# Kernel tuning notes

Hardware: AMD Instinct MI355X
Metric: run time of the kernel (lower is better)

The kernel has to match this reference:

```python
import jax, jax.numpy as jnp
import numpy as np

V, H, B, S = 32000, 2048, 128, 512
NEG_INF = -1e9

def setup_inputs() -> dict:
    key = jax.random.key(0)
    ks = jax.random.split(key, 12)
    sc = 1.0 / np.sqrt(H)
    embed = jax.random.normal(ks[0], (V, H), jnp.float32) * sc
    embed = embed.at[0].set(0.0)  # padding_idx=0
    return {
        "target_words": jax.random.randint(ks[1], (B,), 0, V),
        "hx": jax.random.normal(ks[2], (B, H), jnp.float32),
        "cx": jax.random.normal(ks[3], (B, H), jnp.float32),
        "ew_hx_list": jax.random.normal(ks[4], (S, B, H), jnp.float32),
        "ew_mask": jax.random.randint(ks[5], (S, B, 1), 0, 2).astype(jnp.int32),
        "embed": embed,
        "W_ih": jax.random.normal(ks[6], (4 * H, H), jnp.float32) * sc,
        "W_hh": jax.random.normal(ks[7], (4 * H, H), jnp.float32) * sc,
        "b_ih": jax.random.normal(ks[8], (4 * H,), jnp.float32) * sc,
        "b_hh": jax.random.normal(ks[9], (4 * H,), jnp.float32) * sc,
        "attn_W": jax.random.normal(ks[10], (H, 2 * H), jnp.float32) * sc,
        "attn_b": jax.random.normal(ks[11], (H,), jnp.float32) * sc,
    }

def reference(target_words, hx, cx, ew_hx_list, ew_mask, embed, W_ih, W_hh, b_ih, b_hh, attn_W, attn_b):
    # forward(): embedding (dropout is identity in eval) + LSTMCell step
    x = embed[target_words]                                   # [B,H]
    gates = x @ W_ih.T + b_ih + hx @ W_hh.T + b_hh            # [B,4H]
    i, f, g, o = jnp.split(gates, 4, axis=-1)                 # PyTorch gate order
    i = jax.nn.sigmoid(i); f = jax.nn.sigmoid(f); o = jax.nn.sigmoid(o)
    g = jnp.tanh(g)
    cx_new = f * cx + i * g
    hx_new = o * jnp.tanh(cx_new)                             # [B,H]
    # attention(): masked dot-score softmax over source dim 0
    scores = jnp.sum(hx_new * ew_hx_list, axis=-1, keepdims=True)  # [S,B,1]
    masked = jnp.where(ew_mask == 0, NEG_INF, scores)
    align = jax.nn.softmax(masked, axis=0)                    # [S,B,1]
    content = jnp.sum(align * ew_hx_list, axis=0)             # [B,H]
    concat = jnp.concatenate([content, hx_new], axis=1)       # [B,2H]
    hx_attention = jnp.tanh(concat @ attn_W.T + attn_b)       # [B,H]
    return hx_attention
```

## Files before the change

kernel.cpp:

```cpp
#include <hip/hip_runtime.h>
#include <math.h>

#define B 128
#define H 2048
#define S 512
#define FOURH 8192
#define LOG2E 1.4426950408889634f

typedef float  f32x4  __attribute__((ext_vector_type(4)));
typedef short  bf16x8 __attribute__((ext_vector_type(8)));
typedef unsigned short u16;
typedef unsigned short u16x8 __attribute__((ext_vector_type(8)));
typedef unsigned short u16x4 __attribute__((ext_vector_type(4)));

__device__ __forceinline__ void cvt_hilo(float x, u16& h, u16& lo) {
    unsigned int u = __float_as_uint(x);
    h = (u16)(u >> 16);
    float hf = __uint_as_float(u & 0xFFFF0000u);
    float r = x - hf;
    lo = (u16)(__float_as_uint(r) >> 16);
}

__global__ __launch_bounds__(256) void gather_convert_A0(
    const int* __restrict__ tw,
    const float* __restrict__ embed,
    const float* __restrict__ hx,
    u16* __restrict__ Ah, u16* __restrict__ Al)
{
    const int i = (blockIdx.x * 256 + threadIdx.x) * 8;
    const int b = i >> 12;
    const int col = i & 4095;
    const float* src = (col < H) ? (embed + (size_t)tw[b] * H + col)
                                 : (hx + (size_t)b * H + (col - H));
    f32x4 v0 = *(const f32x4*)(src);
    f32x4 v1 = *(const f32x4*)(src + 4);
    u16x8 hv, lv;
    #pragma unroll
    for (int j = 0; j < 4; ++j) { u16 h, l; cvt_hilo(v0[j], h, l); hv[j] = h; lv[j] = l; }
    #pragma unroll
    for (int j = 0; j < 4; ++j) { u16 h, l; cvt_hilo(v1[j], h, l); hv[4+j] = h; lv[4+j] = l; }
    *(u16x8*)(Ah + i) = hv;
    *(u16x8*)(Al + i) = lv;
}

template<int MODE>
__global__ __launch_bounds__(256) void split_gemm(
    const u16* __restrict__ Ah, const u16* __restrict__ Al,
    const float* __restrict__ W0, const float* __restrict__ W1,
    float* __restrict__ outp)
{
    constexpr int NOUT = (MODE == 0) ? FOURH : H;
    constexpr int KLEN = (MODE == 0) ? 512 : 256;
    constexpr int NITER = KLEN / 32;
    __shared__ u16 AhS[128][40];
    __shared__ u16 AlS[128][40];
    __shared__ u16 BhS[128][40];
    __shared__ u16 BlS[128][40];

    const int tid = threadIdx.x;
    const int n0 = blockIdx.x * 128;
    const int kz = blockIdx.y;
    const int kbase = kz * KLEN;
    const int sr = tid >> 1;
    const int sc = (tid & 1) * 16;
    const int wv = tid >> 6, lane = tid & 63;
    const int wr = (wv >> 1) * 64;
    const int wc = (wv & 1) * 64;
    const int frow = lane & 15, fk = (lane >> 4) * 8, crow = (lane >> 4) * 4;

    const float* Wrow;
    if (MODE == 0)
        Wrow = ((kz < 4) ? W0 : W1) + (size_t)(n0 + sr) * H + (kz & 3) * KLEN + sc;
    else
        Wrow = W0 + (size_t)(n0 + sr) * (2 * H) + kbase + sc;

    const u16* Abase = Ah + (size_t)sr * 4096 + kbase + sc;
    const u16* Lbase = Al + (size_t)sr * 4096 + kbase + sc;

    f32x4 acc[4][4];
    #pragma unroll
    for (int mi = 0; mi < 4; ++mi)
        #pragma unroll
        for (int ni = 0; ni < 4; ++ni)
            acc[mi][ni] = (f32x4){0.f, 0.f, 0.f, 0.f};

    u16x8 rah0, rah1, ral0, ral1;
    auto loadA = [&](int k0) {
        rah0 = *(const u16x8*)(Abase + k0);
        rah1 = *(const u16x8*)(Abase + k0 + 8);
        ral0 = *(const u16x8*)(Lbase + k0);
        ral1 = *(const u16x8*)(Lbase + k0 + 8);
    };
    auto writeA = [&]() {
        *(u16x8*)&AhS[sr][sc]     = rah0;
        *(u16x8*)&AhS[sr][sc + 8] = rah1;
        *(u16x8*)&AlS[sr][sc]     = ral0;
        *(u16x8*)&AlS[sr][sc + 8] = ral1;
    };
    f32x4 wX0, wX1, wX2, wX3, wY0, wY1, wY2, wY3;
    auto loadWX = [&](int k0) {
        wX0 = *(const f32x4*)(Wrow + k0);
        wX1 = *(const f32x4*)(Wrow + k0 + 4);
        wX2 = *(const f32x4*)(Wrow + k0 + 8);
        wX3 = *(const f32x4*)(Wrow + k0 + 12);
    };
    auto loadWY = [&](int k0) {
        wY0 = *(const f32x4*)(Wrow + k0);
        wY1 = *(const f32x4*)(Wrow + k0 + 4);
        wY2 = *(const f32x4*)(Wrow + k0 + 8);
        wY3 = *(const f32x4*)(Wrow + k0 + 12);
    };
    auto writeB = [&](const f32x4& b0, const f32x4& b1,
                      const f32x4& b2, const f32x4& b3) {
        u16x8 hv, lv;
        #pragma unroll
        for (int j = 0; j < 4; ++j) { u16 h, l; cvt_hilo(b0[j], h, l); hv[j] = h; lv[j] = l; }
        #pragma unroll
        for (int j = 0; j < 4; ++j) { u16 h, l; cvt_hilo(b1[j], h, l); hv[4+j] = h; lv[4+j] = l; }
        *(u16x8*)&BhS[sr][sc] = hv;
        *(u16x8*)&BlS[sr][sc] = lv;
        #pragma unroll
        for (int j = 0; j < 4; ++j) { u16 h, l; cvt_hilo(b2[j], h, l); hv[j] = h; lv[j] = l; }
        #pragma unroll
        for (int j = 0; j < 4; ++j) { u16 h, l; cvt_hilo(b3[j], h, l); hv[4+j] = h; lv[4+j] = l; }
        *(u16x8*)&BhS[sr][sc + 8] = hv;
        *(u16x8*)&BlS[sr][sc + 8] = lv;
    };
    auto computeTile = [&]() {
        bf16x8 a_h[4], a_l[4], b_h[4], b_l[4];
        #pragma unroll
        for (int mi = 0; mi < 4; ++mi) {
            a_h[mi] = *(const bf16x8*)&AhS[wr + mi * 16 + frow][fk];
            a_l[mi] = *(const bf16x8*)&AlS[wr + mi * 16 + frow][fk];
        }
        #pragma unroll
        for (int ni = 0; ni < 4; ++ni) {
            b_h[ni] = *(const bf16x8*)&BhS[wc + ni * 16 + frow][fk];
            b_l[ni] = *(const bf16x8*)&BlS[wc + ni * 16 + frow][fk];
        }
        #pragma unroll
        for (int mi = 0; mi < 4; ++mi)
            #pragma unroll
            for (int ni = 0; ni < 4; ++ni) {
                acc[mi][ni] = __builtin_amdgcn_mfma_f32_16x16x32_bf16(a_h[mi], b_h[ni], acc[mi][ni], 0, 0, 0);
                acc[mi][ni] = __builtin_amdgcn_mfma_f32_16x16x32_bf16(a_h[mi], b_l[ni], acc[mi][ni], 0, 0, 0);
                acc[mi][ni] = __builtin_amdgcn_mfma_f32_16x16x32_bf16(a_l[mi], b_h[ni], acc[mi][ni], 0, 0, 0);
            }
    };

    loadWX(0);
    loadWY(32);
    loadA(0);

    for (int ks = 0; ks < NITER; ks += 2) {
        __syncthreads();
        writeA();
        writeB(wX0, wX1, wX2, wX3);
        __syncthreads();
        loadA((ks + 1) * 32);
        if (ks + 2 < NITER) loadWX((ks + 2) * 32);
        computeTile();
        __syncthreads();
        writeA();
        writeB(wY0, wY1, wY2, wY3);
        __syncthreads();
        if (ks + 2 < NITER) loadA((ks + 2) * 32);
        if (ks + 3 < NITER) loadWY((ks + 3) * 32);
        computeTile();
    }

    #pragma unroll
    for (int mi = 0; mi < 4; ++mi)
        #pragma unroll
        for (int ni = 0; ni < 4; ++ni) {
            const int col = n0 + wc + ni * 16 + frow;
            #pragma unroll
            for (int j = 0; j < 4; ++j) {
                const int row = wr + mi * 16 + crow + j;
                outp[((size_t)kz * B + row) * NOUT + col] = acc[mi][ni][j];
            }
        }
}

__global__ __launch_bounds__(256) void lstm_cell(
    const float* __restrict__ gp,
    const float* __restrict__ cx,
    const float* __restrict__ b_ih,
    const float* __restrict__ b_hh,
    float* __restrict__ hxn,
    u16* __restrict__ Ah1, u16* __restrict__ Al1)
{
    const int t = blockIdx.x * 256 + threadIdx.x;
    const int b = t >> 9;
    const int h = (t & 511) * 4;
    const size_t PS = (size_t)B * FOURH;
    const float* g0 = gp + (size_t)b * FOURH;
    f32x4 gi = *(const f32x4*)(b_ih + h)       + *(const f32x4*)(b_hh + h);
    f32x4 gf = *(const f32x4*)(b_ih + H + h)   + *(const f32x4*)(b_hh + H + h);
    f32x4 gg = *(const f32x4*)(b_ih + 2*H + h) + *(const f32x4*)(b_hh + 2*H + h);
    f32x4 go = *(const f32x4*)(b_ih + 3*H + h) + *(const f32x4*)(b_hh + 3*H + h);
    #pragma unroll
    for (int p = 0; p < 8; ++p) {
        gi += *(const f32x4*)(g0 + p * PS + h);
        gf += *(const f32x4*)(g0 + p * PS + H + h);
        gg += *(const f32x4*)(g0 + p * PS + 2*H + h);
        go += *(const f32x4*)(g0 + p * PS + 3*H + h);
    }
    f32x4 cv = *(const f32x4*)(cx + (size_t)b * H + h);
    f32x4 hv;
    #pragma unroll
    for (int j = 0; j < 4; ++j) {
        float i_ = 1.f / (1.f + expf(-gi[j]));
        float f_ = 1.f / (1.f + expf(-gf[j]));
        float o_ = 1.f / (1.f + expf(-go[j]));
        float g_ = tanhf(gg[j]);
        float c_ = f_ * cv[j] + i_ * g_;
        hv[j] = o_ * tanhf(c_);
    }
    *(f32x4*)(hxn + (size_t)b * H + h) = hv;
    u16x4 hh, ll;
    #pragma unroll
    for (int j = 0; j < 4; ++j) { u16 a, l; cvt_hilo(hv[j], a, l); hh[j] = a; ll[j] = l; }
    *(u16x4*)(Ah1 + (size_t)b * 4096 + H + h) = hh;
    *(u16x4*)(Al1 + (size_t)b * 4096 + H + h) = ll;
}

__global__ __launch_bounds__(256) void fused_attn(
    const float* __restrict__ hxn,
    const float* __restrict__ ew,
    const int* __restrict__ mask,
    float* __restrict__ o_part,
    float* __restrict__ ml_part)
{
    __shared__ float mlbuf[4][2];
    __shared__ float obuf[4][2048];

    const int tid = threadIdx.x;
    const int b = blockIdx.x >> 2;
    const int c = blockIdx.x & 3;
    const int wv = tid >> 6;
    const int lane = tid & 63;
    const int s0 = c * 128 + wv * 32;

    unsigned long long mbits;
    {
        int mv = (lane < 32) ? mask[(s0 + lane) * B + b] : 0;
        mbits = __ballot(mv != 0);
    }

    f32x4 hxv[8];
    const float* hp = hxn + (size_t)b * H + lane * 4;
    #pragma unroll
    for (int j = 0; j < 8; ++j) hxv[j] = *(const f32x4*)(hp + j * 256);

    f32x4 o4[8];
    #pragma unroll
    for (int j = 0; j < 8; ++j) o4[j] = (f32x4){0.f, 0.f, 0.f, 0.f};
    float m2 = -3.0e38f, l = 0.f;

    const size_t SSTRIDE = (size_t)B * H;
    const float* rowp = ew + ((size_t)s0 * B + b) * H + lane * 4;

    f32x4 eva[8], evb[8];
    #pragma unroll
    for (int j = 0; j < 8; ++j) eva[j] = *(const f32x4*)(rowp + j * 256);
    #pragma unroll
    for (int j = 0; j < 8; ++j) evb[j] = *(const f32x4*)(rowp + SSTRIDE + j * 256);

    for (int pi = 0; pi < 16; ++pi) {
        f32x4 ca[8], cb[8];
        #pragma unroll
        for (int j = 0; j < 8; ++j) { ca[j] = eva[j]; cb[j] = evb[j]; }
        if (pi < 15) {
            const float* na = rowp + (size_t)(2 * pi + 2) * SSTRIDE;
            const float* nb = rowp + (size_t)(2 * pi + 3) * SSTRIDE;
            #pragma unroll
            for (int j = 0; j < 8; ++j) eva[j] = *(const f32x4*)(na + j * 256);
            #pragma unroll
            for (int j = 0; j < 8; ++j) evb[j] = *(const f32x4*)(nb + j * 256);
        }
        float pa = 0.f, pb = 0.f;
        #pragma unroll
        for (int j = 0; j < 8; ++j) {
            f32x4 ta = ca[j] * hxv[j];
            f32x4 tb = cb[j] * hxv[j];
            pa += ta[0] + ta[1] + ta[2] + ta[3];
            pb += tb[0] + tb[1] + tb[2] + tb[3];
        }
        #pragma unroll
        for (int off = 32; off; off >>= 1) {
            pa += __shfl_xor(pa, off, 64);
            pb += __shfl_xor(pb, off, 64);
        }
        const float p2a = ((mbits >> (2 * pi)) & 1) ? pa * LOG2E : -1.5e9f;
        const float p2b = ((mbits >> (2 * pi + 1)) & 1) ? pb * LOG2E : -1.5e9f;
        const float q = fmaxf(p2a, p2b);
        if (q <= m2) {
            const float ea = exp2f(p2a - m2);
            const float eb = exp2f(p2b - m2);
            l += ea + eb;
            #pragma unroll
            for (int j = 0; j < 8; ++j) o4[j] += ca[j] * ea + cb[j] * eb;
        } else {
            const float sc = exp2f(m2 - q);
            const float ea = exp2f(p2a - q);
            const float eb = exp2f(p2b - q);
            l = l * sc + ea + eb;
            #pragma unroll
            for (int j = 0; j < 8; ++j) o4[j] = o4[j] * sc + ca[j] * ea + cb[j] * eb;
            m2 = q;
        }
    }

    if (lane == 0) { mlbuf[wv][0] = m2; mlbuf[wv][1] = l; }
    __syncthreads();
    const float M = fmaxf(fmaxf(mlbuf[0][0], mlbuf[1][0]), fmaxf(mlbuf[2][0], mlbuf[3][0]));
    const float wsc = exp2f(m2 - M);
    float L = 0.f;
    #pragma unroll
    for (int w = 0; w < 4; ++w) L += mlbuf[w][1] * exp2f(mlbuf[w][0] - M);
    #pragma unroll
    for (int j = 0; j < 8; ++j)
        *(f32x4*)&obuf[wv][j * 256 + lane * 4] = o4[j] * wsc;
    __syncthreads();

    const int h0 = tid * 8;
    f32x4 s0v = (f32x4){0.f, 0.f, 0.f, 0.f}, s1v = s0v;
    #pragma unroll
    for (int w = 0; w < 4; ++w) {
        s0v += *(const f32x4*)&obuf[w][h0];
        s1v += *(const f32x4*)&obuf[w][h0 + 4];
    }
    float* op = o_part + ((size_t)b * 4 + c) * H + h0;
    *(f32x4*)(op)     = s0v;
    *(f32x4*)(op + 4) = s1v;
    if (tid == 0) {
        ml_part[((size_t)b * 4 + c) * 2]     = M;
        ml_part[((size_t)b * 4 + c) * 2 + 1] = L;
    }
}

__global__ __launch_bounds__(256) void attn_combine(
    const float* __restrict__ o_part,
    const float* __restrict__ ml_part,
    u16* __restrict__ Ah1, u16* __restrict__ Al1)
{
    const int b = blockIdx.x;
    const int tid = threadIdx.x;
    float Mc[4], Lc[4];
    #pragma unroll
    for (int c = 0; c < 4; ++c) {
        Mc[c] = ml_part[((size_t)b * 4 + c) * 2];
        Lc[c] = ml_part[((size_t)b * 4 + c) * 2 + 1];
    }
    const float Mg = fmaxf(fmaxf(Mc[0], Mc[1]), fmaxf(Mc[2], Mc[3]));
    float Lg = 0.f;
    #pragma unroll
    for (int c = 0; c < 4; ++c) Lg += Lc[c] * exp2f(Mc[c] - Mg);
    const float inv = 1.f / Lg;
    const int h0 = tid * 8;
    f32x4 a0 = (f32x4){0.f, 0.f, 0.f, 0.f}, a1 = a0;
    #pragma unroll
    for (int c = 0; c < 4; ++c) {
        const float scl = exp2f(Mc[c] - Mg) * inv;
        const float* op = o_part + ((size_t)b * 4 + c) * H + h0;
        a0 += *(const f32x4*)(op) * scl;
        a1 += *(const f32x4*)(op + 4) * scl;
    }
    u16x8 hh, ll;
    #pragma unroll
    for (int j = 0; j < 4; ++j) { u16 a, l; cvt_hilo(a0[j], a, l); hh[j] = a; ll[j] = l; }
    #pragma unroll
    for (int j = 0; j < 4; ++j) { u16 a, l; cvt_hilo(a1[j], a, l); hh[4+j] = a; ll[4+j] = l; }
    *(u16x8*)(Ah1 + (size_t)b * 4096 + h0) = hh;
    *(u16x8*)(Al1 + (size_t)b * 4096 + h0) = ll;
}

__global__ __launch_bounds__(256) void attn_out(
    const float* __restrict__ part,
    const float* __restrict__ attn_b,
    float* __restrict__ out)
{
    const int t = blockIdx.x * 256 + threadIdx.x;
    const int i = t * 4;
    const int n = i & (H - 1);
    const size_t BH = (size_t)B * H;
    f32x4 s = *(const f32x4*)(attn_b + n);
    #pragma unroll
    for (int p = 0; p < 16; ++p) s += *(const f32x4*)(part + p * BH + i);
    f32x4 r;
    #pragma unroll
    for (int j = 0; j < 4; ++j) r[j] = tanhf(s[j]);
    *(f32x4*)(out + i) = r;
}

extern "C" void kernel_launch(void* const* d_in, const int* in_sizes, int n_in,
                              void* d_out, int out_size, void* d_ws, size_t ws_size,
                              hipStream_t stream)
{
    const int*   tw     = (const int*)d_in[0];
    const float* hx     = (const float*)d_in[1];
    const float* cx     = (const float*)d_in[2];
    const float* ew     = (const float*)d_in[3];
    const int*   mask   = (const int*)d_in[4];
    const float* embed  = (const float*)d_in[5];
    const float* W_ih   = (const float*)d_in[6];
    const float* W_hh   = (const float*)d_in[7];
    const float* b_ih   = (const float*)d_in[8];
    const float* b_hh   = (const float*)d_in[9];
    const float* attn_W = (const float*)d_in[10];
    const float* attn_b = (const float*)d_in[11];
    float* out = (float*)d_out;

    float* ws      = (float*)d_ws;
    float* gates_p = ws;
    float* o_part  = gates_p + 8 * (size_t)B * FOURH;
    float* ml      = o_part + (size_t)B * 4 * H;
    float* hxn     = ml + 1024;
    float* out_p   = hxn + (size_t)B * H;
    u16* Ah0 = (u16*)(out_p + 16 * (size_t)B * H);
    u16* Al0 = Ah0 + (size_t)B * 4096;
    u16* Ah1 = Al0 + (size_t)B * 4096;
    u16* Al1 = Ah1 + (size_t)B * 4096;

    gather_convert_A0<<<256, 256, 0, stream>>>(tw, embed, hx, Ah0, Al0);
    split_gemm<0><<<dim3(FOURH / 128, 8), 256, 0, stream>>>(Ah0, Al0, W_ih, W_hh, gates_p);
    lstm_cell<<<256, 256, 0, stream>>>(gates_p, cx, b_ih, b_hh, hxn, Ah1, Al1);
    fused_attn<<<B * 4, 256, 0, stream>>>(hxn, ew, mask, o_part, ml);
    attn_combine<<<B, 256, 0, stream>>>(o_part, ml, Ah1, Al1);
    split_gemm<1><<<dim3(H / 128, 16), 256, 0, stream>>>(Ah1, Al1, attn_W, attn_W, out_p);
    attn_out<<<256, 256, 0, stream>>>(out_p, attn_b, out);
}
```

Measured before the change: 186.0 us.

## Overlap hx-half of attention output GEMM with attention kernel

Splits the output projection GEMM by K: the half that multiplies hx_new (available right after the LSTM cell) is computed by extra blocks appended to the attention kernel, and only the content half runs after attn_combine. This overlaps half of the projection work with the memory-bound attention pass and shrinks the serialized tail GEMM. In exchange the attention kernel's shared memory grows to a shared 41KB buffer, which may lower its occupancy, and the GEMM blocks compete with attention for bandwidth.

```diff
diff --git a/kernel.cpp b/kernel.cpp
--- a/kernel.cpp
+++ b/kernel.cpp
@@ -43,14 +43,12 @@
     *(u16x8*)(Al + i) = lv;
 }
 
-template<int MODE>
-__global__ __launch_bounds__(256) void split_gemm(
+__global__ __launch_bounds__(256) void gates_gemm(
     const u16* __restrict__ Ah, const u16* __restrict__ Al,
     const float* __restrict__ W0, const float* __restrict__ W1,
     float* __restrict__ outp)
 {
-    constexpr int NOUT = (MODE == 0) ? FOURH : H;
-    constexpr int KLEN = (MODE == 0) ? 512 : 256;
+    constexpr int KLEN = 512;
     constexpr int NITER = KLEN / 32;
     __shared__ u16 AhS[128][40];
     __shared__ u16 AlS[128][40];
@@ -68,12 +66,7 @@
     const int wc = (wv & 1) * 64;
     const int frow = lane & 15, fk = (lane >> 4) * 8, crow = (lane >> 4) * 4;
 
-    const float* Wrow;
-    if (MODE == 0)
-        Wrow = ((kz < 4) ? W0 : W1) + (size_t)(n0 + sr) * H + (kz & 3) * KLEN + sc;
-    else
-        Wrow = W0 + (size_t)(n0 + sr) * (2 * H) + kbase + sc;
-
+    const float* Wrow = ((kz < 4) ? W0 : W1) + (size_t)(n0 + sr) * H + (kz & 3) * KLEN + sc;
     const u16* Abase = Ah + (size_t)sr * 4096 + kbase + sc;
     const u16* Lbase = Al + (size_t)sr * 4096 + kbase + sc;
 
@@ -177,7 +170,137 @@
             #pragma unroll
             for (int j = 0; j < 4; ++j) {
                 const int row = wr + mi * 16 + crow + j;
-                outp[((size_t)kz * B + row) * NOUT + col] = acc[mi][ni][j];
+                outp[((size_t)kz * B + row) * FOURH + col] = acc[mi][ni][j];
+            }
+        }
+}
+
+__device__ __forceinline__ void gemm1_tile(
+    unsigned char* smem,
+    const u16* __restrict__ Ah, const u16* __restrict__ Al,
+    const float* __restrict__ attn_W,
+    int n0, int kbase, int kzout, float* __restrict__ outp)
+{
+    constexpr int NITER = 8;
+    typedef u16 (*tile_t)[40];
+    tile_t AhS = (tile_t)(smem);
+    tile_t AlS = (tile_t)(smem + 10240);
+    tile_t BhS = (tile_t)(smem + 20480);
+    tile_t BlS = (tile_t)(smem + 30720);
+
+    const int tid = threadIdx.x;
+    const int sr = tid >> 1;
+    const int sc = (tid & 1) * 16;
+    const int wv = tid >> 6, lane = tid & 63;
+    const int wr = (wv >> 1) * 64;
+    const int wc = (wv & 1) * 64;
+    const int frow = lane & 15, fk = (lane >> 4) * 8, crow = (lane >> 4) * 4;
+
+    const float* Wrow = attn_W + (size_t)(n0 + sr) * (2 * H) + kbase + sc;
+    const u16* Abase = Ah + (size_t)sr * 4096 + kbase + sc;
+    const u16* Lbase = Al + (size_t)sr * 4096 + kbase + sc;
+
+    f32x4 acc[4][4];
+    #pragma unroll
+    for (int mi = 0; mi < 4; ++mi)
+        #pragma unroll
+        for (int ni = 0; ni < 4; ++ni)
+            acc[mi][ni] = (f32x4){0.f, 0.f, 0.f, 0.f};
+
+    u16x8 rah0, rah1, ral0, ral1;
+    auto loadA = [&](int k0) {
+        rah0 = *(const u16x8*)(Abase + k0);
+        rah1 = *(const u16x8*)(Abase + k0 + 8);
+        ral0 = *(const u16x8*)(Lbase + k0);
+        ral1 = *(const u16x8*)(Lbase + k0 + 8);
+    };
+    auto writeA = [&]() {
+        *(u16x8*)&AhS[sr][sc]     = rah0;
+        *(u16x8*)&AhS[sr][sc + 8] = rah1;
+        *(u16x8*)&AlS[sr][sc]     = ral0;
+        *(u16x8*)&AlS[sr][sc + 8] = ral1;
+    };
+    f32x4 wX0, wX1, wX2, wX3, wY0, wY1, wY2, wY3;
+    auto loadWX = [&](int k0) {
+        wX0 = *(const f32x4*)(Wrow + k0);
+        wX1 = *(const f32x4*)(Wrow + k0 + 4);
+        wX2 = *(const f32x4*)(Wrow + k0 + 8);
+        wX3 = *(const f32x4*)(Wrow + k0 + 12);
+    };
+    auto loadWY = [&](int k0) {
+        wY0 = *(const f32x4*)(Wrow + k0);
+        wY1 = *(const f32x4*)(Wrow + k0 + 4);
+        wY2 = *(const f32x4*)(Wrow + k0 + 8);
+        wY3 = *(const f32x4*)(Wrow + k0 + 12);
+    };
+    auto writeB = [&](const f32x4& b0, const f32x4& b1,
+                      const f32x4& b2, const f32x4& b3) {
+        u16x8 hv, lv;
+        #pragma unroll
+        for (int j = 0; j < 4; ++j) { u16 h, l; cvt_hilo(b0[j], h, l); hv[j] = h; lv[j] = l; }
+        #pragma unroll
+        for (int j = 0; j < 4; ++j) { u16 h, l; cvt_hilo(b1[j], h, l); hv[4+j] = h; lv[4+j] = l; }
+        *(u16x8*)&BhS[sr][sc] = hv;
+        *(u16x8*)&BlS[sr][sc] = lv;
+        #pragma unroll
+        for (int j = 0; j < 4; ++j) { u16 h, l; cvt_hilo(b2[j], h, l); hv[j] = h; lv[j] = l; }
+        #pragma unroll
+        for (int j = 0; j < 4; ++j) { u16 h, l; cvt_hilo(b3[j], h, l); hv[4+j] = h; lv[4+j] = l; }
+        *(u16x8*)&BhS[sr][sc + 8] = hv;
+        *(u16x8*)&BlS[sr][sc + 8] = lv;
+    };
+    auto computeTile = [&]() {
+        bf16x8 a_h[4], a_l[4], b_h[4], b_l[4];
+        #pragma unroll
+        for (int mi = 0; mi < 4; ++mi) {
+            a_h[mi] = *(const bf16x8*)&AhS[wr + mi * 16 + frow][fk];
+            a_l[mi] = *(const bf16x8*)&AlS[wr + mi * 16 + frow][fk];
+        }
+        #pragma unroll
+        for (int ni = 0; ni < 4; ++ni) {
+            b_h[ni] = *(const bf16x8*)&BhS[wc + ni * 16 + frow][fk];
+            b_l[ni] = *(const bf16x8*)&BlS[wc + ni * 16 + frow][fk];
+        }
+        #pragma unroll
+        for (int mi = 0; mi < 4; ++mi)
+            #pragma unroll
+            for (int ni = 0; ni < 4; ++ni) {
+                acc[mi][ni] = __builtin_amdgcn_mfma_f32_16x16x32_bf16(a_h[mi], b_h[ni], acc[mi][ni], 0, 0, 0);
+                acc[mi][ni] = __builtin_amdgcn_mfma_f32_16x16x32_bf16(a_h[mi], b_l[ni], acc[mi][ni], 0, 0, 0);
+                acc[mi][ni] = __builtin_amdgcn_mfma_f32_16x16x32_bf16(a_l[mi], b_h[ni], acc[mi][ni], 0, 0, 0);
+            }
+    };
+
+    loadWX(0);
+    loadWY(32);
+    loadA(0);
+
+    for (int ks = 0; ks < NITER; ks += 2) {
+        __syncthreads();
+        writeA();
+        writeB(wX0, wX1, wX2, wX3);
+        __syncthreads();
+        loadA((ks + 1) * 32);
+        if (ks + 2 < NITER) loadWX((ks + 2) * 32);
+        computeTile();
+        __syncthreads();
+        writeA();
+        writeB(wY0, wY1, wY2, wY3);
+        __syncthreads();
+        if (ks + 2 < NITER) loadA((ks + 2) * 32);
+        if (ks + 3 < NITER) loadWY((ks + 3) * 32);
+        computeTile();
+    }
+
+    #pragma unroll
+    for (int mi = 0; mi < 4; ++mi)
+        #pragma unroll
+        for (int ni = 0; ni < 4; ++ni) {
+            const int col = n0 + wc + ni * 16 + frow;
+            #pragma unroll
+            for (int j = 0; j < 4; ++j) {
+                const int row = wr + mi * 16 + crow + j;
+                outp[((size_t)kzout * B + row) * H + col] = acc[mi][ni][j];
             }
         }
 }
@@ -225,15 +348,28 @@
     *(u16x4*)(Al1 + (size_t)b * 4096 + H + h) = ll;
 }
 
-__global__ __launch_bounds__(256) void fused_attn(
+__global__ __launch_bounds__(256) void fused_attn_g1(
     const float* __restrict__ hxn,
     const float* __restrict__ ew,
     const int* __restrict__ mask,
     float* __restrict__ o_part,
-    float* __restrict__ ml_part)
-{
-    __shared__ float mlbuf[4][2];
-    __shared__ float obuf[4][2048];
+    float* __restrict__ ml_part,
+    const u16* __restrict__ Ah1, const u16* __restrict__ Al1,
+    const float* __restrict__ attn_W,
+    float* __restrict__ out_p)
+{
+    __shared__ __align__(16) unsigned char smem[41024];
+
+    if (blockIdx.x >= 512) {
+        const int bid = blockIdx.x - 512;
+        const int n0 = (bid >> 3) * 128;
+        const int kz = bid & 7;
+        gemm1_tile(smem, Ah1, Al1, attn_W, n0, 2048 + kz * 256, 8 + kz, out_p);
+        return;
+    }
+
+    float (*obuf)[2048] = (float(*)[2048])smem;
+    float (*mlbuf)[2]   = (float(*)[2])(smem + 32768);
 
     const int tid = threadIdx.x;
     const int b = blockIdx.x >> 2;
@@ -374,6 +510,17 @@
     for (int j = 0; j < 4; ++j) { u16 a, l; cvt_hilo(a1[j], a, l); hh[4+j] = a; ll[4+j] = l; }
     *(u16x8*)(Ah1 + (size_t)b * 4096 + h0) = hh;
     *(u16x8*)(Al1 + (size_t)b * 4096 + h0) = ll;
+}
+
+__global__ __launch_bounds__(256) void gemm1_content(
+    const u16* __restrict__ Ah1, const u16* __restrict__ Al1,
+    const float* __restrict__ attn_W,
+    float* __restrict__ out_p)
+{
+    __shared__ __align__(16) unsigned char smem[41024];
+    const int n0 = (blockIdx.x >> 3) * 128;
+    const int kz = blockIdx.x & 7;
+    gemm1_tile(smem, Ah1, Al1, attn_W, n0, kz * 256, kz, out_p);
 }
 
 __global__ __launch_bounds__(256) void attn_out(
@@ -424,10 +571,11 @@
     u16* Al1 = Ah1 + (size_t)B * 4096;
 
     gather_convert_A0<<<256, 256, 0, stream>>>(tw, embed, hx, Ah0, Al0);
-    split_gemm<0><<<dim3(FOURH / 128, 8), 256, 0, stream>>>(Ah0, Al0, W_ih, W_hh, gates_p);
+    gates_gemm<<<dim3(FOURH / 128, 8), 256, 0, stream>>>(Ah0, Al0, W_ih, W_hh, gates_p);
     lstm_cell<<<256, 256, 0, stream>>>(gates_p, cx, b_ih, b_hh, hxn, Ah1, Al1);
-    fused_attn<<<B * 4, 256, 0, stream>>>(hxn, ew, mask, o_part, ml);
+    fused_attn_g1<<<512 + 128, 256, 0, stream>>>(hxn, ew, mask, o_part, ml,
+                                                 Ah1, Al1, attn_W, out_p);
     attn_combine<<<B, 256, 0, stream>>>(o_part, ml, Ah1, Al1);
-    split_gemm<1><<<dim3(H / 128, 16), 256, 0, stream>>>(Ah1, Al1, attn_W, attn_W, out_p);
+    gemm1_content<<<128, 256, 0, stream>>>(Ah1, Al1, attn_W, out_p);
     attn_out<<<256, 256, 0, stream>>>(out_p, attn_b, out);
 }
```

After: 190.1 us. +2.2%, slower.
